# Performance work log

Measured on AMD Instinct MI355X. Metric: run time of the kernel, lower is better.

The kernel has to match this reference:

```python
import jax, jax.numpy as jnp
import numpy as np

B, S, D, H = 2, 2048, 1024, 16
HD = D // H          # head_dim = 64
HALF = HD // 2       # rotary pair count = 32


def rope_freqs(seq_len, half, base=10000.0):
    # Llama-style: theta_j = base^(-2j/head_dim), angle m*theta_j
    inv = 1.0 / (base ** (np.arange(0, half, dtype=np.float32) / half))
    ang = np.arange(seq_len, dtype=np.float32)[:, None] * inv[None, :]  # [S, half]
    return jnp.asarray(np.cos(ang)), jnp.asarray(np.sin(ang))


def setup_inputs() -> dict:
    key = jax.random.key(0)
    kx, kq, kk, kv, ko = jax.random.split(key, 5)
    cos, sin = rope_freqs(S, HALF)  # real/imag of m_theta_polar_tensor
    s = 0.02
    return {
        "x": jax.random.normal(kx, (B, S, D), dtype=jnp.float32),
        "freqs_cos": cos,
        "freqs_sin": sin,
        "Wq": jax.random.normal(kq, (D, D), dtype=jnp.float32) * s,
        "Wk": jax.random.normal(kk, (D, D), dtype=jnp.float32) * s,
        "Wv": jax.random.normal(kv, (D, D), dtype=jnp.float32) * s,
        "Wout": jax.random.normal(ko, (D, D), dtype=jnp.float32) * s,
    }


def _apply_rope(t, cos, sin):
    # t: [B, S, H, HD]; rotate consecutive pairs (complex multiply)
    b, s, h, hd = t.shape
    tr = t.reshape(b, s, h, hd // 2, 2)
    t0, t1 = tr[..., 0], tr[..., 1]
    c = cos[None, :, None, :]  # [1, S, 1, HALF]
    sn = sin[None, :, None, :]
    o0 = t0 * c - t1 * sn
    o1 = t0 * sn + t1 * c
    return jnp.stack([o0, o1], axis=-1).reshape(b, s, h, hd)


def reference(x, freqs_cos, freqs_sin, Wq, Wk, Wv, Wout):
    b, s, _ = x.shape
    q = (x @ Wq).reshape(b, s, H, HD)
    k = (x @ Wk).reshape(b, s, H, HD)
    v = (x @ Wv).reshape(b, s, H, HD)
    q = _apply_rope(q, freqs_cos, freqs_sin)
    k = _apply_rope(k, freqs_cos, freqs_sin)
    # [B, H, S, S]
    scores = jnp.einsum("bqhd,bkhd->bhqk", q, k) / jnp.sqrt(jnp.float32(HD))
    causal = jnp.triu(jnp.ones((s, s), dtype=bool), k=1)
    scores = jnp.where(causal[None, None], -jnp.inf, scores)
    weights = jax.nn.softmax(scores, axis=-1)
    vectors = jnp.einsum("bhqk,bkhd->bqhd", weights, v).reshape(b, s, D)
    return vectors @ Wout
```

## Files before the change

kernel.cpp:

```cpp
#include <hip/hip_runtime.h>
#include <stdint.h>

typedef unsigned short u16;
typedef __attribute__((ext_vector_type(8))) short short8;
typedef __attribute__((ext_vector_type(4))) float f32x4;
typedef __attribute__((ext_vector_type(4))) unsigned short ushort4v;
typedef __attribute__((ext_vector_type(2))) unsigned int uint2v;

#define NB 2
#define NS 2048
#define ND 1024
#define NH 16
#define HDIM 64
#define NHALF 32
#define QSCALE 0.18033688f
#define NEGBIG -3.0e38f

__device__ __forceinline__ float bf2f(u16 u) {
  union { unsigned u; float f; } v; v.u = ((unsigned)u) << 16; return v.f;
}
__device__ __forceinline__ u16 f2bf(float f) {
  union { float f; unsigned u; } v; v.f = f;
  unsigned r = v.u + 0x7fffu + ((v.u >> 16) & 1u);
  return (u16)(r >> 16);
}

__device__ __forceinline__ unsigned cvt_pk_bf16(float lo, float hi) {
  unsigned r;
  asm("v_cvt_pk_bf16_f32 %0, %1, %2" : "=v"(r) : "v"(lo), "v"(hi));
  return r;
}

__device__ __forceinline__ void gld_lds16(const u16* g, u16* l) {
  void* gv = (void*)g;
  __builtin_amdgcn_global_load_lds((__attribute__((address_space(1))) void*)gv,
                                   (__attribute__((address_space(3))) void*)l, 16, 0, 0);
}

__global__ void prep(const float* __restrict__ x, u16* __restrict__ xb,
                     const float* __restrict__ W0, const float* __restrict__ W1,
                     const float* __restrict__ W2, const float* __restrict__ W3,
                     u16* __restrict__ dqkv, u16* __restrict__ dout) {
  __shared__ float tile[32][33];
  const int bid = blockIdx.x;
  if (bid < 4096) {
    int i = bid * 256 + threadIdx.x;
    float4 v = ((const float4*)x)[i];
    ushort4v o;
    o.x = f2bf(v.x); o.y = f2bf(v.y); o.z = f2bf(v.z); o.w = f2bf(v.w);
    ((ushort4v*)xb)[i] = o;
  } else {
    int idx = bid - 4096;
    const int z = idx >> 10;
    idx &= 1023;
    const int bx = idx & 31, by = idx >> 5;
    const float* W = (z == 0) ? W0 : (z == 1) ? W1 : (z == 2) ? W2 : W3;
    u16* dst = (z < 3) ? (dqkv + (size_t)z * ND * ND) : dout;
    const int n0 = bx * 32, k0 = by * 32;
    const int tx = threadIdx.x & 31, ty = threadIdx.x >> 5;
#pragma unroll
    for (int i = 0; i < 4; ++i)
      tile[ty + i * 8][tx] = W[(size_t)(k0 + ty + i * 8) * ND + n0 + tx];
    __syncthreads();
#pragma unroll
    for (int i = 0; i < 4; ++i)
      dst[(size_t)(n0 + ty + i * 8) * ND + k0 + tx] = f2bf(tile[tx][ty + i * 8]);
  }
}

template<int MI, int MODE>
__device__ __forceinline__ void gemm_body(
    u16* smem0, int bx, int by,
    const u16* __restrict__ A, const u16* __restrict__ BT,
    u16* __restrict__ qo, u16* __restrict__ ko, u16* __restrict__ vo,
    float* __restrict__ fo,
    const float* __restrict__ cosT, const float* __restrict__ sinT) {
  constexpr int BUFSZ = MI * 2048 + 8192;
  const int tid = threadIdx.x;
  const int w = tid >> 6, lane = tid & 63;
  const int lr = lane & 15, lg = lane >> 4;
  const int bm = by * (MI * 32), bn = bx << 7;
  const int wr = (w >> 1) * (MI * 16), wc = (w & 1) << 6;
  f32x4 acc[MI][4] = {};

  const int arow = tid >> 3;
  const int aslot = (tid & 7) ^ (arow & 7);
  const u16* ags = A + (size_t)(bm + arow) * ND + (aslot << 3);
  const u16* bgs = BT + (size_t)(bn + arow) * ND + (aslot << 3);

  int af_off[MI][2], bf_off[4][2];
#pragma unroll
  for (int mi = 0; mi < MI; ++mi)
#pragma unroll
    for (int kk = 0; kk < 2; ++kk)
      af_off[mi][kk] = (wr + mi * 16 + lr) * 64 + ((((kk << 2) + lg) ^ (lr & 7)) << 3);
#pragma unroll
  for (int ni = 0; ni < 4; ++ni)
#pragma unroll
    for (int kk = 0; kk < 2; ++kk)
      bf_off[ni][kk] = (wc + ni * 16 + lr) * 64 + ((((kk << 2) + lg) ^ (lr & 7)) << 3);

  auto stage = [&](int buf, int kt) {
    u16* dst = smem0 + buf * BUFSZ;
#pragma unroll
    for (int it = 0; it < MI; ++it)
      gld_lds16(ags + it * (32 * ND) + kt, dst + it * 2048 + w * 512);
#pragma unroll
    for (int it = 0; it < 4; ++it)
      gld_lds16(bgs + it * (32 * ND) + kt, dst + MI * 2048 + it * 2048 + w * 512);
  };

  stage(0, 0);
  __syncthreads();
  int cur = 0;
  for (int kt = 0; kt < ND; kt += 64) {
    if (kt + 64 < ND) stage(cur ^ 1, kt + 64);
    const u16* As = smem0 + cur * BUFSZ;
    const u16* Bs = As + MI * 2048;
#pragma unroll
    for (int kk = 0; kk < 2; ++kk) {
      short8 af[MI], bfr[4];
#pragma unroll
      for (int mi = 0; mi < MI; ++mi)
        af[mi] = *(const short8*)(As + af_off[mi][kk]);
#pragma unroll
      for (int ni = 0; ni < 4; ++ni)
        bfr[ni] = *(const short8*)(Bs + bf_off[ni][kk]);
#pragma unroll
      for (int mi = 0; mi < MI; ++mi)
#pragma unroll
        for (int ni = 0; ni < 4; ++ni) {
          if (MODE == 0)
            acc[mi][ni] = __builtin_amdgcn_mfma_f32_16x16x32_bf16(bfr[ni], af[mi], acc[mi][ni], 0, 0, 0);
          else
            acc[mi][ni] = __builtin_amdgcn_mfma_f32_16x16x32_bf16(af[mi], bfr[ni], acc[mi][ni], 0, 0, 0);
        }
    }
    __syncthreads();
    cur ^= 1;
  }

  if (MODE == 0) {
#pragma unroll
    for (int mi = 0; mi < MI; ++mi) {
      const int m = bm + wr + mi * 16 + lr;
      const int b = m >> 11, s = m & 2047;
      const float* cbase = cosT + s * NHALF;
      const float* sbase = sinT + s * NHALF;
#pragma unroll
      for (int ni = 0; ni < 4; ++ni) {
        const int n = bn + wc + ni * 16 + (lg << 2);
        const int which = n >> 10, hh = (n >> 6) & 15, d0 = n & 63;
        u16* dst = which == 0 ? qo : ko;
        const float sc = which == 0 ? QSCALE : 1.0f;
        const float2 cp = *(const float2*)(cbase + (d0 >> 1));
        const float2 sp = *(const float2*)(sbase + (d0 >> 1));
        const float v0 = acc[mi][ni][0], v1 = acc[mi][ni][1];
        const float v2 = acc[mi][ni][2], v3 = acc[mi][ni][3];
        uint2v pk;
        pk.x = cvt_pk_bf16((v0 * cp.x - v1 * sp.x) * sc, (v0 * sp.x + v1 * cp.x) * sc);
        pk.y = cvt_pk_bf16((v2 * cp.y - v3 * sp.y) * sc, (v2 * sp.y + v3 * cp.y) * sc);
        *(uint2v*)(dst + (((size_t)(b * NH + hh) * NS + s) << 6) + d0) = pk;
      }
    }
  } else if (MODE == 1) {
#pragma unroll
    for (int mi = 0; mi < MI; ++mi) {
#pragma unroll
      for (int ni = 0; ni < 4; ++ni) {
        const int n = bn + wc + ni * 16 + lr;
        const int hh = n >> 6, d = n & 63;
        const int m0 = bm + wr + mi * 16 + (lg << 2);
        const int b = m0 >> 11, s0 = m0 & 2047;
        uint2v pk;
        pk.x = cvt_pk_bf16(acc[mi][ni][0], acc[mi][ni][1]);
        pk.y = cvt_pk_bf16(acc[mi][ni][2], acc[mi][ni][3]);
        *(uint2v*)(vo + ((size_t)(b * NH + hh) * HDIM + d) * NS + s0) = pk;
      }
    }
  } else {
#pragma unroll
    for (int mi = 0; mi < MI; ++mi)
#pragma unroll
      for (int ni = 0; ni < 4; ++ni)
#pragma unroll
        for (int j = 0; j < 4; ++j) {
          const int m = bm + wr + mi * 16 + (lg << 2) + j;
          const int n = bn + wc + ni * 16 + lr;
          fo[(size_t)m * ND + n] = acc[mi][ni][j];
        }
  }
}

__global__ __launch_bounds__(256) void gemm_qkv(
    const u16* __restrict__ xb, const u16* __restrict__ WTqkv, const u16* __restrict__ WTv,
    u16* __restrict__ Qb, u16* __restrict__ Kb, u16* __restrict__ VT,
    const float* __restrict__ fc, const float* __restrict__ fs) {
  __shared__ u16 smem[2 * 16384];
  const int bid = blockIdx.x;
  if (bid < 512) {
    gemm_body<4, 0>(smem, bid & 15, bid >> 4, xb, WTqkv, Qb, Kb, nullptr, nullptr, fc, fs);
  } else {
    const int idx = bid - 512;
    gemm_body<2, 1>(smem, idx & 7, idx >> 3, xb, WTv, nullptr, nullptr, VT, nullptr, nullptr, nullptr);
  }
}

__global__ __launch_bounds__(256) void gemm_out_k(
    const u16* __restrict__ Ob, const u16* __restrict__ WTo, float* __restrict__ out) {
  __shared__ u16 smem[2 * 12288];
  gemm_body<2, 2>(smem, blockIdx.x, blockIdx.y, Ob, WTo, nullptr, nullptr, nullptr, out, nullptr, nullptr);
}

__global__ __launch_bounds__(256) void attn_k(
    const u16* __restrict__ Qb, const u16* __restrict__ Kb,
    const u16* __restrict__ VT, u16* __restrict__ Ob) {
  __shared__ u16 K2[2][8192];
  __shared__ u16 V2[2][8192];
  __shared__ u16 Pl[4][2048];
  const int tid = threadIdx.x, w = tid >> 6, lane = tid & 63;
  const int lr = lane & 15, lg = lane >> 4;
  const int bid = blockIdx.x;
  const int xcd = bid & 7, i = bid >> 3;
  const int bh = xcd * 4 + (i & 3);
  const int pair = i >> 2;
  const int b = bh >> 4, h = bh & 15;
  const u16* Qp = Qb + (size_t)bh * NS * HDIM;
  const u16* Kp = Kb + (size_t)bh * NS * HDIM;
  const u16* Vp = VT + (size_t)bh * NS * HDIM;

  int kf_off[8][2], vb_off[4][4], pw_off[8], pa_off[4];
#pragma unroll
  for (int u = 0; u < 8; ++u) {
    const int kvr = (u << 4) + lr;
#pragma unroll
    for (int c = 0; c < 2; ++c)
      kf_off[u][c] = kvr * 64 + ((((c << 6) + (lg << 4)) ^ ((kvr & 7) << 4)) >> 1);
  }
#pragma unroll
  for (int dn = 0; dn < 4; ++dn) {
    const int d = (dn << 4) + lr;
#pragma unroll
    for (int ks = 0; ks < 4; ++ks)
      vb_off[dn][ks] = d * 128 + ((((ks << 6) + (lg << 4)) ^ ((d & 15) << 4)) >> 1);
  }
#pragma unroll
  for (int u = 0; u < 8; ++u)
    pw_off[u] = lr * 128 + ((((u << 5) + (lg << 3)) ^ ((lr & 15) << 4)) >> 1);
#pragma unroll
  for (int ks = 0; ks < 4; ++ks)
    pa_off[ks] = lr * 128 + ((((ks << 6) + (lg << 4)) ^ ((lr & 15) << 4)) >> 1);
  u16* Pw = &Pl[w][0];

  const int rr = tid >> 3, slot = tid & 7;
  const int ksoff = ((slot ^ (rr & 7)) << 3);
  const u16* kg = Kp + (size_t)rr * HDIM + ksoff;
  const int vr = tid >> 4, vslot = tid & 15;
  const int vsoff = ((vslot ^ vr) << 3);
  const u16* vg = Vp + (size_t)vr * NS + vsoff;

#define STAGE(BUFI, KV0)                                                            \
  {                                                                                 \
    _Pragma("unroll")                                                               \
    for (int c = 0; c < 4; ++c) {                                                   \
      gld_lds16(kg + (size_t)((KV0) + c * 32) * HDIM, &K2[BUFI][c * 2048 + w * 512]); \
      gld_lds16(vg + (size_t)(c * 16) * NS + (KV0),   &V2[BUFI][c * 2048 + w * 512]); \
    }                                                                               \
  }

#define STEP(BUF, KVT)                                                            \
  {                                                                               \
    const int kv0 = (KVT) << 7;                                                   \
    if ((KVT) + 1 < nst) STAGE(BUF ^ 1, kv0 + 128);                               \
    const u16* Kl = K2[BUF];                                                      \
    const u16* Vl = V2[BUF];                                                      \
    f32x4 st[8] = {};                                                             \
    __builtin_amdgcn_s_setprio(1);                                                \
    _Pragma("unroll") for (int u = 0; u < 8; ++u)                                 \
      _Pragma("unroll") for (int c = 0; c < 2; ++c)                               \
        st[u] = __builtin_amdgcn_mfma_f32_16x16x32_bf16(                          \
            *(const short8*)(Kl + kf_off[u][c]), qf[c], st[u], 0, 0, 0);          \
    __builtin_amdgcn_s_setprio(0);                                                \
    if (kv0 + 127 > qw) {                                                         \
      _Pragma("unroll") for (int u = 0; u < 8; ++u)                               \
        _Pragma("unroll") for (int j = 0; j < 4; ++j) {                           \
          const int kvg = kv0 + (u << 4) + (lg << 2) + j;                         \
          if (kvg > q_col) st[u][j] = NEGBIG;                                     \
        }                                                                         \
    }                                                                             \
    _Pragma("unroll") for (int u = 0; u < 8; ++u) {                               \
      const float e0 = __builtin_amdgcn_exp2f(st[u][0]);                          \
      const float e1 = __builtin_amdgcn_exp2f(st[u][1]);                          \
      const float e2 = __builtin_amdgcn_exp2f(st[u][2]);                          \
      const float e3 = __builtin_amdgcn_exp2f(st[u][3]);                          \
      lacc += (e0 + e1) + (e2 + e3);                                              \
      uint2v pk;                                                                  \
      pk.x = cvt_pk_bf16(e0, e1);                                                 \
      pk.y = cvt_pk_bf16(e2, e3);                                                 \
      *(uint2v*)(Pw + pw_off[u]) = pk;                                            \
    }                                                                             \
    {                                                                             \
      short8 pa[4];                                                               \
      _Pragma("unroll") for (int ks = 0; ks < 4; ++ks)                            \
        pa[ks] = *(const short8*)(Pw + pa_off[ks]);                               \
      __builtin_amdgcn_s_setprio(1);                                              \
      _Pragma("unroll") for (int dn = 0; dn < 4; ++dn)                            \
        _Pragma("unroll") for (int ks = 0; ks < 4; ++ks)                          \
          o[dn] = __builtin_amdgcn_mfma_f32_16x16x32_bf16(                        \
              pa[ks], *(const short8*)(Vl + vb_off[dn][ks]), o[dn], 0, 0, 0);     \
      __builtin_amdgcn_s_setprio(0);                                              \
    }                                                                             \
    __syncthreads();                                                              \
  }

  for (int seg = 0; seg < 2; ++seg) {
    const int tile = seg ? pair : 31 - pair;
    const int q0 = tile << 6;
    const int qw = q0 + w * 16;
    const int q_col = qw + lr;
    const int nst = (tile + 2) >> 1;

    short8 qf[2];
#pragma unroll
    for (int c = 0; c < 2; ++c)
      qf[c] = *(const short8*)(Qp + (size_t)(qw + lr) * HDIM + c * 32 + lg * 8);

    f32x4 o[4] = {};
    float lacc = 0.f;

    STAGE(0, 0);
    __syncthreads();

    int kvt = 0;
    for (; kvt + 2 <= nst; kvt += 2) {
      STEP(0, kvt);
      STEP(1, kvt + 1);
    }
    if (kvt < nst) STEP(0, kvt);

    float rs = lacc;
    rs += __shfl_xor(rs, 16);
    rs += __shfl_xor(rs, 32);
    float li[4];
#pragma unroll
    for (int j = 0; j < 4; ++j) li[j] = 1.0f / __shfl(rs, (lg << 2) + j);
#pragma unroll
    for (int dn = 0; dn < 4; ++dn)
#pragma unroll
      for (int j = 0; j < 4; ++j) {
        const int m = b * NS + qw + (lg << 2) + j;
        const int col = h * 64 + dn * 16 + lr;
        Ob[(size_t)m * ND + col] = f2bf(o[dn][j] * li[j]);
      }
  }
}

extern "C" void kernel_launch(void* const* d_in, const int* in_sizes, int n_in,
                              void* d_out, int out_size, void* d_ws, size_t ws_size,
                              hipStream_t stream) {
  const float* x  = (const float*)d_in[0];
  const float* fc = (const float*)d_in[1];
  const float* fs = (const float*)d_in[2];
  const float* Wq = (const float*)d_in[3];
  const float* Wk = (const float*)d_in[4];
  const float* Wv = (const float*)d_in[5];
  const float* Wo = (const float*)d_in[6];
  float* out = (float*)d_out;
  char* ws = (char*)d_ws;

  u16* xb    = (u16*)(ws);
  u16* Ob    = (u16*)(ws);
  u16* WTqkv = (u16*)(ws + (size_t)(8u << 20));
  u16* WTo   = (u16*)(ws + (size_t)(14u << 20));
  u16* Qb    = (u16*)(ws + (size_t)(16u << 20));
  u16* Kb    = (u16*)(ws + (size_t)(24u << 20));
  u16* VT    = (u16*)(ws + (size_t)(32u << 20));
  u16* WTv   = WTqkv + (size_t)2 * ND * ND;

  prep<<<8192, 256, 0, stream>>>(x, xb, Wq, Wk, Wv, Wo, WTqkv, WTo);
  gemm_qkv<<<1024, 256, 0, stream>>>(xb, WTqkv, WTv, Qb, Kb, VT, fc, fs);
  attn_k<<<512, 256, 0, stream>>>(Qb, Kb, VT, Ob);
  gemm_out_k<<<dim3(8, 64), 256, 0, stream>>>(Ob, WTo, out);
}
```

Measured before the change: 100.0 us.

## Fuse x fp32-to-bf16 conversion into QKV GEMM A-tile loading

```diff
diff --git a/kernel.cpp b/kernel.cpp
--- a/kernel.cpp
+++ b/kernel.cpp
@@ -37,45 +37,37 @@
                                    (__attribute__((address_space(3))) void*)l, 16, 0, 0);
 }
 
-__global__ void prep(const float* __restrict__ x, u16* __restrict__ xb,
-                     const float* __restrict__ W0, const float* __restrict__ W1,
-                     const float* __restrict__ W2, const float* __restrict__ W3,
-                     u16* __restrict__ dqkv, u16* __restrict__ dout) {
+__global__ void prep_w(const float* __restrict__ W0, const float* __restrict__ W1,
+                       const float* __restrict__ W2, const float* __restrict__ W3,
+                       u16* __restrict__ dqkv, u16* __restrict__ dout) {
   __shared__ float tile[32][33];
-  const int bid = blockIdx.x;
-  if (bid < 4096) {
-    int i = bid * 256 + threadIdx.x;
-    float4 v = ((const float4*)x)[i];
-    ushort4v o;
-    o.x = f2bf(v.x); o.y = f2bf(v.y); o.z = f2bf(v.z); o.w = f2bf(v.w);
-    ((ushort4v*)xb)[i] = o;
-  } else {
-    int idx = bid - 4096;
-    const int z = idx >> 10;
-    idx &= 1023;
-    const int bx = idx & 31, by = idx >> 5;
-    const float* W = (z == 0) ? W0 : (z == 1) ? W1 : (z == 2) ? W2 : W3;
-    u16* dst = (z < 3) ? (dqkv + (size_t)z * ND * ND) : dout;
-    const int n0 = bx * 32, k0 = by * 32;
-    const int tx = threadIdx.x & 31, ty = threadIdx.x >> 5;
-#pragma unroll
-    for (int i = 0; i < 4; ++i)
-      tile[ty + i * 8][tx] = W[(size_t)(k0 + ty + i * 8) * ND + n0 + tx];
-    __syncthreads();
-#pragma unroll
-    for (int i = 0; i < 4; ++i)
-      dst[(size_t)(n0 + ty + i * 8) * ND + k0 + tx] = f2bf(tile[tx][ty + i * 8]);
-  }
+  int idx = blockIdx.x;
+  const int z = idx >> 10;
+  idx &= 1023;
+  const int bx = idx & 31, by = idx >> 5;
+  const float* W = (z == 0) ? W0 : (z == 1) ? W1 : (z == 2) ? W2 : W3;
+  u16* dst = (z < 3) ? (dqkv + (size_t)z * ND * ND) : dout;
+  const int n0 = bx * 32, k0 = by * 32;
+  const int tx = threadIdx.x & 31, ty = threadIdx.x >> 5;
+#pragma unroll
+  for (int i = 0; i < 4; ++i)
+    tile[ty + i * 8][tx] = W[(size_t)(k0 + ty + i * 8) * ND + n0 + tx];
+  __syncthreads();
+#pragma unroll
+  for (int i = 0; i < 4; ++i)
+    dst[(size_t)(n0 + ty + i * 8) * ND + k0 + tx] = f2bf(tile[tx][ty + i * 8]);
 }
 
 template<int MI, int MODE>
 __device__ __forceinline__ void gemm_body(
     u16* smem0, int bx, int by,
-    const u16* __restrict__ A, const u16* __restrict__ BT,
+    const float* __restrict__ Xf, const u16* __restrict__ A,
+    const u16* __restrict__ BT,
     u16* __restrict__ qo, u16* __restrict__ ko, u16* __restrict__ vo,
     float* __restrict__ fo,
     const float* __restrict__ cosT, const float* __restrict__ sinT) {
   constexpr int BUFSZ = MI * 2048 + 8192;
+  constexpr int LA = MI * 2;
   const int tid = threadIdx.x;
   const int w = tid >> 6, lane = tid & 63;
   const int lr = lane & 15, lg = lane >> 4;
@@ -85,8 +77,10 @@
 
   const int arow = tid >> 3;
   const int aslot = (tid & 7) ^ (arow & 7);
-  const u16* ags = A + (size_t)(bm + arow) * ND + (aslot << 3);
   const u16* bgs = BT + (size_t)(bn + arow) * ND + (aslot << 3);
+  const u16* ags = (MODE == 2) ? (A + (size_t)(bm + arow) * ND + (aslot << 3)) : nullptr;
+  const float* axs = (MODE != 2)
+      ? (Xf + (size_t)(bm + (tid >> 4)) * ND + ((tid & 15) << 2)) : nullptr;
 
   int af_off[MI][2], bf_off[4][2];
 #pragma unroll
@@ -100,21 +94,54 @@
     for (int kk = 0; kk < 2; ++kk)
       bf_off[ni][kk] = (wc + ni * 16 + lr) * 64 + ((((kk << 2) + lg) ^ (lr & 7)) << 3);
 
-  auto stage = [&](int buf, int kt) {
+  float4 areg[LA];
+  auto loadA = [&](int kt) {
+#pragma unroll
+    for (int i = 0; i < LA; ++i)
+      areg[i] = *(const float4*)(axs + (size_t)i * 16 * ND + kt);
+  };
+  auto writeA = [&](int buf) {
+    u16* dst = smem0 + buf * BUFSZ;
+    const int g = tid & 15;
+    const int slotbase = g >> 1;
+    const int hoff = (g & 1) * 4;
+#pragma unroll
+    for (int i = 0; i < LA; ++i) {
+      const int row = i * 16 + (tid >> 4);
+      const int slot = slotbase ^ (row & 7);
+      uint2v pk;
+      pk.x = cvt_pk_bf16(areg[i].x, areg[i].y);
+      pk.y = cvt_pk_bf16(areg[i].z, areg[i].w);
+      *(uint2v*)(dst + row * 64 + slot * 8 + hoff) = pk;
+    }
+  };
+  auto stageB = [&](int buf, int kt) {
+    u16* dst = smem0 + buf * BUFSZ + MI * 2048;
+#pragma unroll
+    for (int it = 0; it < 4; ++it)
+      gld_lds16(bgs + it * (32 * ND) + kt, dst + it * 2048 + w * 512);
+  };
+  auto stageA16 = [&](int buf, int kt) {
     u16* dst = smem0 + buf * BUFSZ;
 #pragma unroll
     for (int it = 0; it < MI; ++it)
       gld_lds16(ags + it * (32 * ND) + kt, dst + it * 2048 + w * 512);
-#pragma unroll
-    for (int it = 0; it < 4; ++it)
-      gld_lds16(bgs + it * (32 * ND) + kt, dst + MI * 2048 + it * 2048 + w * 512);
   };
 
-  stage(0, 0);
+  if constexpr (MODE != 2) loadA(0);
+  stageB(0, 0);
+  if constexpr (MODE == 2) stageA16(0, 0);
+  if constexpr (MODE != 2) writeA(0);
   __syncthreads();
+
   int cur = 0;
   for (int kt = 0; kt < ND; kt += 64) {
-    if (kt + 64 < ND) stage(cur ^ 1, kt + 64);
+    const bool more = kt + 64 < ND;
+    if (more) {
+      if constexpr (MODE != 2) loadA(kt + 64);
+      stageB(cur ^ 1, kt + 64);
+      if constexpr (MODE == 2) stageA16(cur ^ 1, kt + 64);
+    }
     const u16* As = smem0 + cur * BUFSZ;
     const u16* Bs = As + MI * 2048;
 #pragma unroll
@@ -136,6 +163,7 @@
             acc[mi][ni] = __builtin_amdgcn_mfma_f32_16x16x32_bf16(af[mi], bfr[ni], acc[mi][ni], 0, 0, 0);
         }
     }
+    if (more) { if constexpr (MODE != 2) writeA(cur ^ 1); }
     __syncthreads();
     cur ^= 1;
   }
@@ -193,23 +221,28 @@
 }
 
 __global__ __launch_bounds__(256) void gemm_qkv(
-    const u16* __restrict__ xb, const u16* __restrict__ WTqkv, const u16* __restrict__ WTv,
+    const float* __restrict__ x, const u16* __restrict__ WTqkv, const u16* __restrict__ WTv,
     u16* __restrict__ Qb, u16* __restrict__ Kb, u16* __restrict__ VT,
     const float* __restrict__ fc, const float* __restrict__ fs) {
   __shared__ u16 smem[2 * 16384];
   const int bid = blockIdx.x;
   if (bid < 512) {
-    gemm_body<4, 0>(smem, bid & 15, bid >> 4, xb, WTqkv, Qb, Kb, nullptr, nullptr, fc, fs);
+    const int bx = ((bid & 7) << 1) | ((bid >> 3) & 1);
+    const int by = bid >> 4;
+    gemm_body<4, 0>(smem, bx, by, x, nullptr, WTqkv, Qb, Kb, nullptr, nullptr, fc, fs);
   } else {
     const int idx = bid - 512;
-    gemm_body<2, 1>(smem, idx & 7, idx >> 3, xb, WTv, nullptr, nullptr, VT, nullptr, nullptr, nullptr);
+    gemm_body<2, 1>(smem, idx & 7, idx >> 3, x, nullptr, WTv,
+                    nullptr, nullptr, VT, nullptr, nullptr, nullptr);
   }
 }
 
 __global__ __launch_bounds__(256) void gemm_out_k(
     const u16* __restrict__ Ob, const u16* __restrict__ WTo, float* __restrict__ out) {
   __shared__ u16 smem[2 * 12288];
-  gemm_body<2, 2>(smem, blockIdx.x, blockIdx.y, Ob, WTo, nullptr, nullptr, nullptr, out, nullptr, nullptr);
+  const int bid = blockIdx.x;
+  gemm_body<2, 2>(smem, bid & 7, bid >> 3, nullptr, Ob, WTo,
+                  nullptr, nullptr, nullptr, out, nullptr, nullptr);
 }
 
 __global__ __launch_bounds__(256) void attn_k(
@@ -368,7 +401,6 @@
   float* out = (float*)d_out;
   char* ws = (char*)d_ws;
 
-  u16* xb    = (u16*)(ws);
   u16* Ob    = (u16*)(ws);
   u16* WTqkv = (u16*)(ws + (size_t)(8u << 20));
   u16* WTo   = (u16*)(ws + (size_t)(14u << 20));
@@ -377,8 +409,8 @@
   u16* VT    = (u16*)(ws + (size_t)(32u << 20));
   u16* WTv   = WTqkv + (size_t)2 * ND * ND;
 
-  prep<<<8192, 256, 0, stream>>>(x, xb, Wq, Wk, Wv, Wo, WTqkv, WTo);
-  gemm_qkv<<<1024, 256, 0, stream>>>(xb, WTqkv, WTv, Qb, Kb, VT, fc, fs);
+  prep_w<<<4096, 256, 0, stream>>>(Wq, Wk, Wv, Wo, WTqkv, WTo);
+  gemm_qkv<<<1024, 256, 0, stream>>>(x, WTqkv, WTv, Qb, Kb, VT, fc, fs);
   attn_k<<<512, 256, 0, stream>>>(Qb, Kb, VT, Ob);
-  gemm_out_k<<<dim3(8, 64), 256, 0, stream>>>(Ob, WTo, out);
-}
+  gemm_out_k<<<512, 256, 0, stream>>>(Ob, WTo, out);
+}
```

New measurement: 116.2 us. +16.2%, slower.
